# Kernel optimization log

Hardware: AMD Instinct MI355X
Metric: run time of the kernel (lower is better)

## Reference

```python
import jax, jax.numpy as jnp
import numpy as np

N_NODES = 50000
N_EDGES = 800000
N_RELS = 8
D = 64


def setup_inputs() -> dict:
    key = jax.random.key(0)
    ks = jax.random.split(key, 8)
    h = jax.random.normal(ks[0], (N_NODES, D), dtype=jnp.float32)
    norm = jax.random.uniform(ks[1], (N_EDGES, 1), dtype=jnp.float32)
    W = jax.random.normal(ks[2], (N_RELS, D, D), dtype=jnp.float32) * (1.0 / np.sqrt(D))
    loop_weight = jax.random.normal(ks[3], (D, D), dtype=jnp.float32) * (1.0 / np.sqrt(D))
    h_bias = jnp.zeros((D,), dtype=jnp.float32)
    src = jax.random.randint(ks[4], (N_EDGES,), 0, N_NODES, dtype=jnp.int32)
    dst = jax.random.randint(ks[5], (N_EDGES,), 0, N_NODES, dtype=jnp.int32)
    r = jax.random.randint(ks[6], (N_EDGES,), 0, N_RELS, dtype=jnp.int32)
    return {"h": h, "norm": norm, "W": W, "loop_weight": loop_weight,
            "h_bias": h_bias, "src": src, "dst": dst, "r": r}


def reference(h, norm, W, loop_weight, h_bias, src, dst, r):
    n_nodes = h.shape[0]
    # Precompute h @ W[k] for every relation, then gather per edge.
    # hw: (N, K, D_out) -- cheaper than materializing per-edge (E, D, D) weights.
    hw = jnp.einsum('nd,kdo->nko', h, W)
    msg = hw[src, r] * norm                       # (E, D_out)
    agg = jax.ops.segment_sum(msg, dst, num_segments=n_nodes)  # scatter-sum
    loop_message = h @ loop_weight                # self-loop matmul (dropout=0)
    node_repr = agg + h_bias + loop_message
    return jax.nn.relu(node_repr)
```

## Files before the change

### kernel.cpp

```cpp
#include <hip/hip_runtime.h>

#define N_NODES 50000
#define N_EDGES 800000
#define N_RELS  8
#define NCOL    576
#define MAXDEG  64
#define BPACK_ELEMS (NCOL * 64)

typedef __attribute__((ext_vector_type(8))) short short8;
typedef __attribute__((ext_vector_type(4))) float f32x4;

static __device__ __forceinline__ short f2bf(float f) {
    unsigned u = __float_as_uint(f);
    unsigned r = (u + 0x7FFFu + ((u >> 16) & 1u)) >> 16;
    return (short)r;
}
static __device__ __forceinline__ float bf2f(unsigned short b) {
    return __uint_as_float(((unsigned)b) << 16);
}

__global__ __launch_bounds__(256) void k_bpack(const float* __restrict__ W,
                                               const float* __restrict__ lw,
                                               unsigned short* __restrict__ Bpack,
                                               int* __restrict__ cnt) {
    const int id = blockIdx.x * 256 + threadIdx.x;
    if (id < N_NODES) cnt[id] = 0;
    if (id >= BPACK_ELEMS) return;
    const int e    = id & 7;
    const int lane = (id >> 3) & 63;
    const int g    = id >> 9;
    const int w    = g / 18;
    const int r18  = g - w * 18;
    const int t    = r18 >> 1;
    const int s    = r18 & 1;
    const int c0   = w * 144 + t * 16;
    const int rel  = c0 >> 6;
    const int cc   = (c0 & 63) + (lane & 15);
    const int kk   = s * 32 + (lane >> 4) * 8 + e;
    const float* Bp = (rel < 8) ? (W + (size_t)rel * 4096) : lw;
    Bpack[id] = (unsigned short)f2bf(Bp[(size_t)kk * 64 + cc]);
}

__global__ __launch_bounds__(256) void k_hwfill(const float* __restrict__ h,
                                                const unsigned short* __restrict__ Bpack,
                                                unsigned short* __restrict__ hw2,
                                                const int* __restrict__ src,
                                                const int* __restrict__ dst,
                                                const int* __restrict__ rel,
                                                const float* __restrict__ norm,
                                                int* __restrict__ cnt,
                                                int2* __restrict__ payload) {
    const int e  = blockIdx.x * 256 + threadIdx.x;
    const int sv = src[e];
    const int dv = dst[e];
    const int rv = rel[e];
    const float nv = norm[e];
    const int pos = atomicAdd(&cnt[dv], 1) & (MAXDEG - 1);

    const int lane  = threadIdx.x & 63;
    const int w     = threadIdx.x >> 6;
    const int l15   = lane & 15;
    const int lg    = lane >> 4;
    const int wcol0 = w * 144;
    const int n0    = blockIdx.x * 16;

    short8 barr[9][2];
#pragma unroll
    for (int t = 0; t < 9; ++t)
#pragma unroll
        for (int s = 0; s < 2; ++s)
            barr[t][s] = *(const short8*)(Bpack + ((size_t)(w * 18 + t * 2 + s) * 64 + lane) * 8);

    short8 afr[2];
    const float* hp = h + (size_t)(n0 + l15) * 64 + lg * 8;
#pragma unroll
    for (int s = 0; s < 2; ++s) {
        const float4 x = *(const float4*)(hp + s * 32);
        const float4 y = *(const float4*)(hp + s * 32 + 4);
        short8 a;
        a[0] = f2bf(x.x); a[1] = f2bf(x.y); a[2] = f2bf(x.z); a[3] = f2bf(x.w);
        a[4] = f2bf(y.x); a[5] = f2bf(y.y); a[6] = f2bf(y.z); a[7] = f2bf(y.w);
        afr[s] = a;
    }

    f32x4 acc[9];
#pragma unroll
    for (int t = 0; t < 9; ++t) {
        f32x4 c = {0.f, 0.f, 0.f, 0.f};
        c = __builtin_amdgcn_mfma_f32_16x16x32_bf16(afr[0], barr[t][0], c, 0, 0, 0);
        c = __builtin_amdgcn_mfma_f32_16x16x32_bf16(afr[1], barr[t][1], c, 0, 0, 0);
        acc[t] = c;
    }

    payload[(size_t)dv * MAXDEG + pos] = make_int2(sv * 9 + rv, __float_as_int(nv));

    __shared__ unsigned short lds[16 * NCOL];
#pragma unroll
    for (int t = 0; t < 9; ++t) {
        const int c = wcol0 + t * 16 + l15;
#pragma unroll
        for (int r = 0; r < 4; ++r) {
            const int row = lg * 4 + r;
            lds[row * NCOL + (c ^ (lg << 4))] = (unsigned short)f2bf(acc[t][r]);
        }
    }
    __syncthreads();

    const unsigned* ldsu = (const unsigned*)lds;
    unsigned* outu = (unsigned*)hw2;
#pragma unroll
    for (int i = threadIdx.x; i < 16 * 288; i += 256) {
        const int row = i / 288;
        const int cu  = i - row * 288;
        outu[(size_t)(n0 + row) * 288 + cu] = ldsu[row * 288 + (cu ^ ((row >> 2) << 3))];
    }
}

__global__ __launch_bounds__(256) void k_gather(const unsigned short* __restrict__ hw2,
                                                const int* __restrict__ cnt,
                                                const int2* __restrict__ payload,
                                                const float* __restrict__ bias,
                                                float* __restrict__ out) {
    const int lane = threadIdx.x & 63;
    const int n = (blockIdx.x * 256 + threadIdx.x) >> 6;
    if (n >= N_NODES) return;
    const int deg = min(cnt[n], MAXDEG);
    const int2* pl  = payload + (size_t)n * MAXDEG;
    const int4* pl4 = (const int4*)pl;

    float a0 = bias[lane] + bf2f(hw2[(size_t)n * NCOL + 512 + lane]);
    float a1 = 0.f, a2 = 0.f, a3 = 0.f;
    int t = 0;
    for (; t + 8 <= deg; t += 8) {
        const int4 q0 = pl4[(t >> 1) + 0];
        const int4 q1 = pl4[(t >> 1) + 1];
        const int4 q2 = pl4[(t >> 1) + 2];
        const int4 q3 = pl4[(t >> 1) + 3];
        const float v0 = bf2f(hw2[(size_t)q0.x * 64 + lane]);
        const float v1 = bf2f(hw2[(size_t)q0.z * 64 + lane]);
        const float v2 = bf2f(hw2[(size_t)q1.x * 64 + lane]);
        const float v3 = bf2f(hw2[(size_t)q1.z * 64 + lane]);
        const float v4 = bf2f(hw2[(size_t)q2.x * 64 + lane]);
        const float v5 = bf2f(hw2[(size_t)q2.z * 64 + lane]);
        const float v6 = bf2f(hw2[(size_t)q3.x * 64 + lane]);
        const float v7 = bf2f(hw2[(size_t)q3.z * 64 + lane]);
        a0 += v0 * __int_as_float(q0.y);
        a1 += v1 * __int_as_float(q0.w);
        a2 += v2 * __int_as_float(q1.y);
        a3 += v3 * __int_as_float(q1.w);
        a0 += v4 * __int_as_float(q2.y);
        a1 += v5 * __int_as_float(q2.w);
        a2 += v6 * __int_as_float(q3.y);
        a3 += v7 * __int_as_float(q3.w);
    }
    for (; t + 2 <= deg; t += 2) {
        const int4 q = pl4[t >> 1];
        a0 += bf2f(hw2[(size_t)q.x * 64 + lane]) * __int_as_float(q.y);
        a1 += bf2f(hw2[(size_t)q.z * 64 + lane]) * __int_as_float(q.w);
    }
    if (t < deg) {
        const int2 p = pl[t];
        a0 += bf2f(hw2[(size_t)p.x * 64 + lane]) * __int_as_float(p.y);
    }
    out[(size_t)n * 64 + lane] = fmaxf((a0 + a1) + (a2 + a3), 0.f);
}

__global__ __launch_bounds__(256) void k_edge_direct(const float* __restrict__ h,
                                                     const float* __restrict__ W,
                                                     const int* __restrict__ src,
                                                     const int* __restrict__ dst,
                                                     const int* __restrict__ rel,
                                                     const float* __restrict__ norm,
                                                     float* __restrict__ agg) {
    const int lane  = threadIdx.x & 63;
    const int warp  = (blockIdx.x * 256 + threadIdx.x) >> 6;
    const int nwarp = (gridDim.x * 256) >> 6;
    for (int e = warp; e < N_EDGES; e += nwarp) {
        const int   s  = src[e];
        const int   d2 = dst[e];
        const int   rr = rel[e];
        const float nm = norm[e];
        const float4* hp = (const float4*)(h + (size_t)s * 64);
        const float*  Wr = W + (size_t)rr * 4096;
        float acc = 0.f;
#pragma unroll
        for (int q = 0; q < 16; ++q) {
            float4 hv = hp[q];
            acc += hv.x * Wr[(4 * q + 0) * 64 + lane];
            acc += hv.y * Wr[(4 * q + 1) * 64 + lane];
            acc += hv.z * Wr[(4 * q + 2) * 64 + lane];
            acc += hv.w * Wr[(4 * q + 3) * 64 + lane];
        }
        atomicAdd(&agg[(size_t)d2 * 64 + lane], acc * nm);
    }
}

__global__ __launch_bounds__(256) void k_final(float* __restrict__ out,
                                               const float* __restrict__ h,
                                               const float* __restrict__ lw,
                                               const float* __restrict__ bias) {
    __shared__ float lws[4096];
    for (int i = threadIdx.x; i < 4096; i += 256) lws[i] = lw[i];
    __syncthreads();
    const int lane  = threadIdx.x & 63;
    const int warp  = (blockIdx.x * 256 + threadIdx.x) >> 6;
    const int nwarp = (gridDim.x * 256) >> 6;
    const float b = bias[lane];
    for (int n = warp; n < N_NODES; n += nwarp) {
        const float4* hp = (const float4*)(h + (size_t)n * 64);
        float acc = b;
#pragma unroll
        for (int q = 0; q < 16; ++q) {
            float4 hv = hp[q];
            acc += hv.x * lws[(4 * q + 0) * 64 + lane];
            acc += hv.y * lws[(4 * q + 1) * 64 + lane];
            acc += hv.z * lws[(4 * q + 2) * 64 + lane];
            acc += hv.w * lws[(4 * q + 3) * 64 + lane];
        }
        const size_t idx = (size_t)n * 64 + lane;
        const float v = out[idx] + acc;
        out[idx] = v > 0.f ? v : 0.f;
    }
}

extern "C" void kernel_launch(void* const* d_in, const int* in_sizes, int n_in,
                              void* d_out, int out_size, void* d_ws, size_t ws_size,
                              hipStream_t stream) {
    const float* h    = (const float*)d_in[0];
    const float* norm = (const float*)d_in[1];
    const float* W    = (const float*)d_in[2];
    const float* lw   = (const float*)d_in[3];
    const float* bias = (const float*)d_in[4];
    const int*   src  = (const int*)d_in[5];
    const int*   dst  = (const int*)d_in[6];
    const int*   rel  = (const int*)d_in[7];
    float* out = (float*)d_out;

    char* ws = (char*)d_ws;
    unsigned short* hw2 = (unsigned short*)ws;
    int2* payload = (int2*)(ws + (size_t)N_NODES * NCOL * 2);
    int*  cnt     = (int*)(payload + (size_t)N_NODES * MAXDEG);
    unsigned short* Bpack = (unsigned short*)(cnt + N_NODES + 16);
    const size_t need = (size_t)((char*)(Bpack + BPACK_ELEMS) - ws);

    if (ws_size >= need) {
        k_bpack<<<196, 256, 0, stream>>>(W, lw, Bpack, cnt);
        k_hwfill<<<N_NODES / 16, 256, 0, stream>>>(h, Bpack, hw2, src, dst, rel, norm,
                                                   cnt, payload);
        k_gather<<<(N_NODES + 3) / 4, 256, 0, stream>>>(hw2, cnt, payload, bias, out);
    } else {
        hipMemsetAsync(out, 0, (size_t)out_size * sizeof(float), stream);
        k_edge_direct<<<2048, 256, 0, stream>>>(h, W, src, dst, rel, norm, out);
        k_final<<<1024, 256, 0, stream>>>(out, h, lw, bias);
    }
}
```

Baseline: 82.27 us.

## Replace global per-node atomic edge binning with two-pass bucketed counting sort

Edge bucketing is pulled out of the hw matmul kernel. It becomes two kernels: first a coarse binning of edges into 64-node buckets, using shared-memory histograms and one global atomic per bucket per block, then a per-bucket shared-memory sort into the per-node payload. This replaces 800K global atomics on a 50K counter array with mostly LDS atomics, and it gives the payload writes better locality. The cost is two extra launches, an intermediate buffer that is written and read back, and a per-bucket capacity clamp that could drop edges if a bucket overflows.

```diff
diff --git a/kernel.cpp b/kernel.cpp
--- a/kernel.cpp
+++ b/kernel.cpp
@@ -6,6 +6,13 @@
 #define NCOL    576
 #define MAXDEG  64
 #define BPACK_ELEMS (NCOL * 64)
+#define NTILE   (N_NODES / 16)
+
+#define NBUK    782
+#define BUKCAP  1280
+#define ABLK    256
+#define ATHR    512
+#define ACHUNK  3125
 
 typedef __attribute__((ext_vector_type(8))) short short8;
 typedef __attribute__((ext_vector_type(4))) float f32x4;
@@ -22,9 +29,9 @@
 __global__ __launch_bounds__(256) void k_bpack(const float* __restrict__ W,
                                                const float* __restrict__ lw,
                                                unsigned short* __restrict__ Bpack,
-                                               int* __restrict__ cnt) {
+                                               int* __restrict__ gcnt) {
     const int id = blockIdx.x * 256 + threadIdx.x;
-    if (id < N_NODES) cnt[id] = 0;
+    if (id < NBUK) gcnt[id] = 0;
     if (id >= BPACK_ELEMS) return;
     const int e    = id & 7;
     const int lane = (id >> 3) & 63;
@@ -41,22 +48,9 @@
     Bpack[id] = (unsigned short)f2bf(Bp[(size_t)kk * 64 + cc]);
 }
 
-__global__ __launch_bounds__(256) void k_hwfill(const float* __restrict__ h,
-                                                const unsigned short* __restrict__ Bpack,
-                                                unsigned short* __restrict__ hw2,
-                                                const int* __restrict__ src,
-                                                const int* __restrict__ dst,
-                                                const int* __restrict__ rel,
-                                                const float* __restrict__ norm,
-                                                int* __restrict__ cnt,
-                                                int2* __restrict__ payload) {
-    const int e  = blockIdx.x * 256 + threadIdx.x;
-    const int sv = src[e];
-    const int dv = dst[e];
-    const int rv = rel[e];
-    const float nv = norm[e];
-    const int pos = atomicAdd(&cnt[dv], 1) & (MAXDEG - 1);
-
+__global__ __launch_bounds__(256) void k_hw(const float* __restrict__ h,
+                                            const unsigned short* __restrict__ Bpack,
+                                            unsigned short* __restrict__ hw2) {
     const int lane  = threadIdx.x & 63;
     const int w     = threadIdx.x >> 6;
     const int l15   = lane & 15;
@@ -92,8 +86,6 @@
         acc[t] = c;
     }
 
-    payload[(size_t)dv * MAXDEG + pos] = make_int2(sv * 9 + rv, __float_as_int(nv));
-
     __shared__ unsigned short lds[16 * NCOL];
 #pragma unroll
     for (int t = 0; t < 9; ++t) {
@@ -113,6 +105,64 @@
         const int row = i / 288;
         const int cu  = i - row * 288;
         outu[(size_t)(n0 + row) * 288 + cu] = ldsu[row * 288 + (cu ^ ((row >> 2) << 3))];
+    }
+}
+
+__global__ __launch_bounds__(ATHR) void k_abin(const int* __restrict__ src,
+                                               const int* __restrict__ dst,
+                                               const int* __restrict__ rel,
+                                               const float* __restrict__ norm,
+                                               int* __restrict__ gcnt,
+                                               int2* __restrict__ bedges) {
+    __shared__ int lcnt[NBUK], lbase[NBUK], lpos[NBUK];
+    for (int i = threadIdx.x; i < NBUK; i += ATHR) { lcnt[i] = 0; lpos[i] = 0; }
+    __syncthreads();
+
+    const int e0 = blockIdx.x * ACHUNK;
+    for (int e = e0 + threadIdx.x; e < e0 + ACHUNK; e += ATHR)
+        atomicAdd(&lcnt[dst[e] >> 6], 1);
+    __syncthreads();
+
+    for (int i = threadIdx.x; i < NBUK; i += ATHR)
+        lbase[i] = atomicAdd(&gcnt[i], lcnt[i]);
+    __syncthreads();
+
+    for (int e = e0 + threadIdx.x; e < e0 + ACHUNK; e += ATHR) {
+        const int dv  = dst[e];
+        const int bkt = dv >> 6;
+        int idx = lbase[bkt] + atomicAdd(&lpos[bkt], 1);
+        idx = min(idx, BUKCAP - 1);
+        bedges[(size_t)bkt * BUKCAP + idx] =
+            make_int2(((dv & 63) << 19) | (src[e] * 9 + rel[e]),
+                      __float_as_int(norm[e]));
+    }
+}
+
+__global__ __launch_bounds__(256) void k_bsort(const int2* __restrict__ bedges,
+                                               const int* __restrict__ gcnt,
+                                               int2* __restrict__ payload,
+                                               int* __restrict__ cnt) {
+    __shared__ int lc[64];
+    if (threadIdx.x < 64) lc[threadIdx.x] = 0;
+    __syncthreads();
+
+    const int b     = blockIdx.x;
+    const int nb    = min(gcnt[b], BUKCAP);
+    const int nbase = b * 64;
+    const int2* be  = bedges + (size_t)b * BUKCAP;
+
+    for (int i = threadIdx.x; i < nb; i += 256) {
+        const int2 r = be[i];
+        const int  d = (unsigned)r.x >> 19;
+        const int  pos = atomicAdd(&lc[d], 1) & (MAXDEG - 1);
+        payload[(size_t)(nbase + d) * MAXDEG + pos] =
+            make_int2(r.x & 0x7FFFF, r.y);
+    }
+    __syncthreads();
+
+    if (threadIdx.x < 64) {
+        const int n = nbase + threadIdx.x;
+        if (n < N_NODES) cnt[n] = lc[threadIdx.x];
     }
 }
 
@@ -238,15 +288,18 @@
 
     char* ws = (char*)d_ws;
     unsigned short* hw2 = (unsigned short*)ws;
-    int2* payload = (int2*)(ws + (size_t)N_NODES * NCOL * 2);
-    int*  cnt     = (int*)(payload + (size_t)N_NODES * MAXDEG);
+    int2* bedges  = (int2*)(ws + (size_t)N_NODES * NCOL * 2);
+    int2* payload = bedges + (size_t)NBUK * BUKCAP;
+    int*  gcnt    = (int*)(payload + (size_t)N_NODES * MAXDEG);
+    int*  cnt     = gcnt + NBUK + 16;
     unsigned short* Bpack = (unsigned short*)(cnt + N_NODES + 16);
     const size_t need = (size_t)((char*)(Bpack + BPACK_ELEMS) - ws);
 
     if (ws_size >= need) {
-        k_bpack<<<196, 256, 0, stream>>>(W, lw, Bpack, cnt);
-        k_hwfill<<<N_NODES / 16, 256, 0, stream>>>(h, Bpack, hw2, src, dst, rel, norm,
-                                                   cnt, payload);
+        k_bpack<<<196, 256, 0, stream>>>(W, lw, Bpack, gcnt);
+        k_hw<<<NTILE, 256, 0, stream>>>(h, Bpack, hw2);
+        k_abin<<<ABLK, ATHR, 0, stream>>>(src, dst, rel, norm, gcnt, bedges);
+        k_bsort<<<NBUK, 256, 0, stream>>>(bedges, gcnt, payload, cnt);
         k_gather<<<(N_NODES + 3) / 4, 256, 0, stream>>>(hw2, cnt, payload, bias, out);
     } else {
         hipMemsetAsync(out, 0, (size_t)out_size * sizeof(float), stream);
```

After: 82.45 us. Within noise of the previous version (+0.2%).
